# Optimization experiments

Hardware: AMD Instinct MI355X
Metric: run time of the kernel (lower is better)

Reference implementation:

```python
import jax, jax.numpy as jnp
import numpy as np

QK_DIM = 1024
V_DIM = 1024
NUM_HEADS = 16
HEAD_DIM = 64
INNER = NUM_HEADS * HEAD_DIM  # 1024
SCALE = HEAD_DIM ** -0.5


def setup_inputs() -> dict:
    key = jax.random.key(0)
    ks = jax.random.split(key, 8)
    m, nq, nkv = 4, 2048, 2048
    xq = jax.random.normal(ks[0], (m, nq, QK_DIM), dtype=jnp.float32)
    xk = jax.random.normal(ks[1], (m, nkv, QK_DIM), dtype=jnp.float32)
    xv = jax.random.normal(ks[2], (m, nkv, V_DIM), dtype=jnp.float32)
    # torch nn.Linear weights are [out, in]; y = x @ W.T
    s_qk = (QK_DIM) ** -0.5
    s_in = (INNER) ** -0.5
    Wq = jax.random.uniform(ks[3], (INNER, QK_DIM), jnp.float32, -s_qk, s_qk)
    Wk = jax.random.uniform(ks[4], (INNER, QK_DIM), jnp.float32, -s_qk, s_qk)
    Wv = jax.random.uniform(ks[5], (INNER, V_DIM), jnp.float32, -s_qk, s_qk)
    Wo = jax.random.uniform(ks[6], (V_DIM, INNER), jnp.float32, -s_in, s_in)
    bo = jax.random.uniform(ks[7], (V_DIM,), jnp.float32, -s_in, s_in)
    return {"xq": xq, "xk": xk, "xv": xv, "Wq": Wq, "Wk": Wk, "Wv": Wv, "Wo": Wo, "bo": bo}


def reference(xq, xk, xv, Wq, Wk, Wv, Wo, bo):
    m, nq, _ = xq.shape
    nkv = xk.shape[1]
    # projections (no bias), split heads: b n (h d) -> b h n d
    q = (xq @ Wq.T).reshape(m, nq, NUM_HEADS, HEAD_DIM).transpose(0, 2, 1, 3)
    k = (xk @ Wk.T).reshape(m, nkv, NUM_HEADS, HEAD_DIM).transpose(0, 2, 1, 3)
    v = (xv @ Wv.T).reshape(m, nkv, NUM_HEADS, HEAD_DIM).transpose(0, 2, 1, 3)
    dots = jnp.einsum("bhqd,bhkd->bhqk", q, k) * SCALE  # [m,h,nq,nkv]
    attn = jax.nn.softmax(dots, axis=-1)
    out = jnp.einsum("bhqk,bhkd->bhqd", attn, v)
    out = out.transpose(0, 2, 1, 3).reshape(m, nq, INNER)  # b h n d -> b n (h d)
    return out @ Wo.T + bo  # to_out Linear (dropout p=0 -> identity)
```

## Files before the change

### kernel.cpp

```cpp
#include <hip/hip_runtime.h>

typedef unsigned short u16;
using bf16x8 = __attribute__((ext_vector_type(8))) __bf16;
using f32x4  = __attribute__((ext_vector_type(4))) float;

#define QSCALE 0.18033688011f

#define EXP2F(x) __builtin_amdgcn_exp2f(x)

__device__ __forceinline__ u16 f2bf(float f) {
  union { float f; unsigned int u; } x; x.f = f;
  unsigned int r = x.u + 0x7FFFu + ((x.u >> 16) & 1u);
  return (u16)(r >> 16);
}

__device__ __forceinline__ bf16x8 ld8(const u16* p) {
  return *reinterpret_cast<const bf16x8*>(p);
}

__device__ __forceinline__ void gload16(const u16* g, u16* l) {
  __builtin_amdgcn_global_load_lds(
      (const __attribute__((address_space(1))) unsigned int*)g,
      (__attribute__((address_space(3))) unsigned int*)l, 16, 0, 0);
}

__global__ void cast3_f32_to_bf16(const float* __restrict__ a, const float* __restrict__ b,
                                  const float* __restrict__ c, u16* __restrict__ out, int n4) {
  const int y = blockIdx.y;
  const int i = blockIdx.x * 256 + threadIdx.x;
  if (i >= n4) return;
  const float* src = (y == 0) ? a : (y == 1) ? b : c;
  const float4 v = reinterpret_cast<const float4*>(src)[i];
  ushort4 o;
  o.x = f2bf(v.x); o.y = f2bf(v.y); o.z = f2bf(v.z); o.w = f2bf(v.w);
  reinterpret_cast<ushort4*>(out + (size_t)y * n4 * 4)[i] = o;
}

__global__ void cast4_f32_to_bf16(const float* __restrict__ a, const float* __restrict__ b,
                                  const float* __restrict__ c, const float* __restrict__ d,
                                  u16* __restrict__ out, int n4) {
  const int y = blockIdx.y;
  const int i = blockIdx.x * 256 + threadIdx.x;
  if (i >= n4) return;
  const float* src = (y == 0) ? a : (y == 1) ? b : (y == 2) ? c : d;
  const float4 v = reinterpret_cast<const float4*>(src)[i];
  ushort4 o;
  o.x = f2bf(v.x); o.y = f2bf(v.y); o.z = f2bf(v.z); o.w = f2bf(v.w);
  reinterpret_cast<ushort4*>(out + (size_t)y * n4 * 4)[i] = o;
}

#define GEMM_CORE(A_, B_, K_, BX_, BY_)                                              \
  __shared__ alignas(16) u16 lds_a[128 * 32];                                        \
  __shared__ alignas(16) u16 lds_b[128 * 32];                                        \
  const int t = threadIdx.x;                                                         \
  const int w = t >> 6, lane = t & 63;                                               \
  const int wr = w >> 1, wc = w & 1;                                                 \
  const size_t row0 = (size_t)(BY_) * 128;                                           \
  const size_t col0 = (size_t)(BX_) * 128;                                           \
  f32x4 acc[4][4];                                                                   \
  _Pragma("unroll") for (int i = 0; i < 4; ++i)                                      \
    _Pragma("unroll") for (int j = 0; j < 4; ++j) acc[i][j] = {0.f, 0.f, 0.f, 0.f};  \
  const u16* ga = A_ + (row0 + (t >> 2)) * K_ + (t & 3) * 8;                         \
  const u16* gb = B_ + (col0 + (t >> 2)) * K_ + (t & 3) * 8;                         \
  u16* la = lds_a + w * 512;                                                         \
  u16* lb = lds_b + w * 512;                                                         \
  const int fr = lane & 15;                                                          \
  const int fk = (lane >> 4) * 8;                                                    \
  for (int kt = 0; kt < K_; kt += 32) {                                              \
    __syncthreads();                                                                 \
    gload16(ga + kt, la);                                                            \
    gload16(ga + (size_t)64 * K_ + kt, la + 2048);                                   \
    gload16(gb + kt, lb);                                                            \
    gload16(gb + (size_t)64 * K_ + kt, lb + 2048);                                   \
    __syncthreads();                                                                 \
    bf16x8 af[4], bfr[4];                                                            \
    _Pragma("unroll") for (int i = 0; i < 4; ++i)                                    \
      af[i] = ld8(&lds_a[(wr * 64 + i * 16 + fr) * 32 + fk]);                        \
    _Pragma("unroll") for (int j = 0; j < 4; ++j)                                    \
      bfr[j] = ld8(&lds_b[(wc * 64 + j * 16 + fr) * 32 + fk]);                       \
    _Pragma("unroll") for (int i = 0; i < 4; ++i)                                    \
      _Pragma("unroll") for (int j = 0; j < 4; ++j)                                  \
        acc[i][j] = __builtin_amdgcn_mfma_f32_16x16x32_bf16(af[i], bfr[j], acc[i][j], 0, 0, 0); \
  }                                                                                  \
  const int er = (lane >> 4) * 4, ec = lane & 15;

__global__ __launch_bounds__(256)
void gemm_qkv(const u16* __restrict__ Aall, const u16* __restrict__ Ball,
              u16* __restrict__ Call) {
  const int g = (blockIdx.x & 7) * 192 + (blockIdx.x >> 3);
  const int bx = g & 7, by = (g >> 3) & 63, z = g >> 9;
  const u16* A = Aall + (size_t)z * 8192 * 1024;
  const u16* B = Ball + (size_t)z * 1024 * 1024;
  u16* C = Call + (size_t)z * 8192 * 1024;
  GEMM_CORE(A, B, 1024, bx, by)
#pragma unroll
  for (int i = 0; i < 4; ++i)
#pragma unroll
    for (int j = 0; j < 4; ++j) {
      const size_t row = row0 + wr * 64 + i * 16 + er;
      const size_t col = col0 + wc * 64 + j * 16 + ec;
      if (z == 0) {
#pragma unroll
        for (int r = 0; r < 4; ++r)
          C[(row + r) * 1024 + col] = f2bf(acc[i][j][r] * QSCALE);
      } else if (z == 1) {
#pragma unroll
        for (int r = 0; r < 4; ++r)
          C[(row + r) * 1024 + col] = f2bf(acc[i][j][r]);
      } else {
        ushort4 o4;
        o4.x = f2bf(acc[i][j][0]); o4.y = f2bf(acc[i][j][1]);
        o4.z = f2bf(acc[i][j][2]); o4.w = f2bf(acc[i][j][3]);
        const size_t nloc = row & 2047;
        const size_t pos = (nloc & ~(size_t)31) | (((nloc >> 2) & 3) << 3) |
                           (((nloc >> 4) & 1) << 2) | (nloc & 3);
        const size_t idx = (((row >> 11) * 16 + (col >> 6)) * 64 + (col & 63)) * 2048 + pos;
        *reinterpret_cast<ushort4*>(&C[idx]) = o4;
      }
    }
}

__global__ __launch_bounds__(256)
void gemm_out(const u16* __restrict__ A, const u16* __restrict__ B,
              float* __restrict__ Cf, const float* __restrict__ bias) {
  const int g = (blockIdx.x & 7) * 64 + (blockIdx.x >> 3);
  const int bx = g & 7, by = g >> 3;
  GEMM_CORE(A, B, 1024, bx, by)
#pragma unroll
  for (int i = 0; i < 4; ++i)
#pragma unroll
    for (int j = 0; j < 4; ++j) {
      const size_t row = row0 + wr * 64 + i * 16 + er;
      const size_t col = col0 + wc * 64 + j * 16 + ec;
#pragma unroll
      for (int r = 0; r < 4; ++r)
        Cf[(row + r) * 1024 + col] = acc[i][j][r] + bias[col];
    }
}

__global__ __launch_bounds__(256)
void flash_attn(const u16* __restrict__ Q, const u16* __restrict__ Km,
                const u16* __restrict__ Vt, u16* __restrict__ O) {
  const int o_blk = (blockIdx.x & 7) * 128 + (blockIdx.x >> 3);
  const int qt = o_blk & 15, h = (o_blk >> 4) & 15, b = o_blk >> 8;
  const int t = threadIdx.x;
  const int w = t >> 6, lane = t & 63;
  const int l16 = lane & 15, lh = lane >> 4;

  __shared__ alignas(16) u16 kt_lds[2][64][72];
  __shared__ alignas(16) u16 vt_lds[2][64][72];

  const size_t base_qk = ((size_t)b * 2048) * 1024 + (size_t)h * 64;
  const size_t base_vt = ((size_t)(b * 16 + h)) * 64 * 2048;

  bf16x8 qf[2][2];
#pragma unroll
  for (int g = 0; g < 2; ++g) {
    const size_t qrow = (size_t)qt * 128 + (w * 2 + g) * 16 + l16;
    const u16* qp = Q + base_qk + qrow * 1024 + lh * 8;
    qf[g][0] = ld8(qp);
    qf[g][1] = ld8(qp + 32);
  }

  bf16x8 vones;
#pragma unroll
  for (int i = 0; i < 8; ++i) vones[i] = (__bf16)1.0f;

  f32x4 o_acc[2][4];
  f32x4 o_sum[2];
#pragma unroll
  for (int g = 0; g < 2; ++g) {
#pragma unroll
    for (int j = 0; j < 4; ++j) o_acc[g][j] = {0.f, 0.f, 0.f, 0.f};
    o_sum[g] = {0.f, 0.f, 0.f, 0.f};
  }

  const int sr = t >> 2;
  const int sc = (t & 3) * 16;
  const u16* kg = Km + base_qk + (size_t)sr * 1024 + sc;
  const u16* vg = Vt + base_vt + (size_t)sr * 2048 + sc;

  {
    uint4 k0 = *reinterpret_cast<const uint4*>(kg);
    uint4 k1 = *reinterpret_cast<const uint4*>(kg + 8);
    uint4 v0 = *reinterpret_cast<const uint4*>(vg);
    uint4 v1 = *reinterpret_cast<const uint4*>(vg + 8);
    *reinterpret_cast<uint4*>(&kt_lds[0][sr][sc]) = k0;
    *reinterpret_cast<uint4*>(&kt_lds[0][sr][sc + 8]) = k1;
    *reinterpret_cast<uint4*>(&vt_lds[0][sr][sc]) = v0;
    *reinterpret_cast<uint4*>(&vt_lds[0][sr][sc + 8]) = v1;
  }

  for (int it = 0; it < 32; ++it) {
    const int cur = it & 1;
    __syncthreads();

    const int nkv = ((it + 1) & 31) * 64;
    const u16* kp = kg + (size_t)nkv * 1024;
    uint4 kr0 = *reinterpret_cast<const uint4*>(kp);
    uint4 kr1 = *reinterpret_cast<const uint4*>(kp + 8);
    uint4 vr0 = *reinterpret_cast<const uint4*>(vg + nkv);
    uint4 vr1 = *reinterpret_cast<const uint4*>(vg + nkv + 8);

    f32x4 s[2][4];
#pragma unroll
    for (int g = 0; g < 2; ++g)
#pragma unroll
      for (int j = 0; j < 4; ++j) s[g][j] = {0.f, 0.f, 0.f, 0.f};
    __builtin_amdgcn_s_setprio(1);
#pragma unroll
    for (int j = 0; j < 4; ++j)
#pragma unroll
      for (int ks = 0; ks < 2; ++ks) {
        bf16x8 kf = ld8(&kt_lds[cur][j * 16 + l16][ks * 32 + lh * 8]);
        s[0][j] = __builtin_amdgcn_mfma_f32_16x16x32_bf16(kf, qf[0][ks], s[0][j], 0, 0, 0);
        s[1][j] = __builtin_amdgcn_mfma_f32_16x16x32_bf16(kf, qf[1][ks], s[1][j], 0, 0, 0);
      }
    __builtin_amdgcn_s_setprio(0);

    bf16x8 pa[2][2];
#pragma unroll
    for (int g = 0; g < 2; ++g)
#pragma unroll
      for (int j = 0; j < 4; ++j)
#pragma unroll
        for (int r = 0; r < 4; ++r)
          s[g][j][r] = EXP2F(s[g][j][r]);
#pragma unroll
    for (int g = 0; g < 2; ++g)
#pragma unroll
      for (int c = 0; c < 2; ++c)
#pragma unroll
        for (int i = 0; i < 8; ++i)
          pa[g][c][i] = (__bf16)s[g][2 * c + (i >> 2)][i & 3];

    __builtin_amdgcn_s_setprio(1);
#pragma unroll
    for (int c = 0; c < 2; ++c) {
      o_sum[0] = __builtin_amdgcn_mfma_f32_16x16x32_bf16(pa[0][c], vones, o_sum[0], 0, 0, 0);
      o_sum[1] = __builtin_amdgcn_mfma_f32_16x16x32_bf16(pa[1][c], vones, o_sum[1], 0, 0, 0);
#pragma unroll
      for (int jd = 0; jd < 4; ++jd) {
        bf16x8 vf = ld8(&vt_lds[cur][jd * 16 + l16][c * 32 + lh * 8]);
        o_acc[0][jd] = __builtin_amdgcn_mfma_f32_16x16x32_bf16(pa[0][c], vf, o_acc[0][jd], 0, 0, 0);
        o_acc[1][jd] = __builtin_amdgcn_mfma_f32_16x16x32_bf16(pa[1][c], vf, o_acc[1][jd], 0, 0, 0);
      }
    }
    __builtin_amdgcn_s_setprio(0);

    *reinterpret_cast<uint4*>(&kt_lds[cur ^ 1][sr][sc]) = kr0;
    *reinterpret_cast<uint4*>(&kt_lds[cur ^ 1][sr][sc + 8]) = kr1;
    *reinterpret_cast<uint4*>(&vt_lds[cur ^ 1][sr][sc]) = vr0;
    *reinterpret_cast<uint4*>(&vt_lds[cur ^ 1][sr][sc + 8]) = vr1;
  }

#pragma unroll
  for (int g = 0; g < 2; ++g) {
    float linv[4];
#pragma unroll
    for (int r = 0; r < 4; ++r) linv[r] = 1.0f / o_sum[g][r];
    const size_t orow0 = (size_t)b * 2048 + (size_t)qt * 128 + (w * 2 + g) * 16;
#pragma unroll
    for (int jd = 0; jd < 4; ++jd) {
      const int col = h * 64 + jd * 16 + l16;
#pragma unroll
      for (int r = 0; r < 4; ++r)
        O[(orow0 + lh * 4 + r) * 1024 + col] = f2bf(o_acc[g][jd][r] * linv[r]);
    }
  }
}

extern "C" void kernel_launch(void* const* d_in, const int* in_sizes, int n_in,
                              void* d_out, int out_size, void* d_ws, size_t ws_size,
                              hipStream_t stream) {
  const float* xq = (const float*)d_in[0];
  const float* xk = (const float*)d_in[1];
  const float* xv = (const float*)d_in[2];
  const float* Wq = (const float*)d_in[3];
  const float* Wk = (const float*)d_in[4];
  const float* Wv = (const float*)d_in[5];
  const float* Wo = (const float*)d_in[6];
  const float* bo = (const float*)d_in[7];
  float* out = (float*)d_out;

  const size_t X = (size_t)8192 * 1024;
  const size_t W = (size_t)1024 * 1024;

  u16* p = (u16*)d_ws;
  u16* x_bf  = p; p += 3 * X;
  u16* w_bf  = p; p += 4 * W;
  u16* qkv   = p; p += 3 * X;
  u16* attn_bf = x_bf;

  dim3 blk(256);
  cast3_f32_to_bf16<<<dim3(8192, 3), blk, 0, stream>>>(xq, xk, xv, x_bf, (int)(X / 4));
  cast4_f32_to_bf16<<<dim3(1024, 4), blk, 0, stream>>>(Wq, Wk, Wv, Wo, w_bf, (int)(W / 4));

  gemm_qkv<<<dim3(1536), blk, 0, stream>>>(x_bf, w_bf, qkv);

  flash_attn<<<dim3(1024), blk, 0, stream>>>(qkv, qkv + X, qkv + 2 * X, attn_bf);

  gemm_out<<<dim3(512), blk, 0, stream>>>(attn_bf, w_bf + 3 * W, out, bo);
}
```

Measured before the change: 213.8 us.

## Use async global-to-LDS loads with XOR-swizzled K/V layout and larger attention blocks

The QKV GEMM epilogue now writes K and transposed V with an XOR swizzle on the 8-element chunk index. This lets flash attention fill unpadded LDS tiles with direct global_load_lds copies and still read them without bank conflicts. The old register-staged prefetch and LDS store are dropped. Attention blocks grow to 512 threads covering 256 query rows, halving the grid so each K/V tile is reused across more queries, at the cost of fewer blocks and heavier per-block sync.

```diff
diff --git a/kernel.cpp b/kernel.cpp
--- a/kernel.cpp
+++ b/kernel.cpp
@@ -105,16 +105,22 @@
           C[(row + r) * 1024 + col] = f2bf(acc[i][j][r] * QSCALE);
       } else if (z == 1) {
 #pragma unroll
-        for (int r = 0; r < 4; ++r)
-          C[(row + r) * 1024 + col] = f2bf(acc[i][j][r]);
+        for (int r = 0; r < 4; ++r) {
+          const size_t n = row + r;
+          const size_t colswz = (col & ~(size_t)63) |
+                                ((col & 63) ^ (((n & 7) << 3)));
+          C[n * 1024 + colswz] = f2bf(acc[i][j][r]);
+        }
       } else {
         ushort4 o4;
         o4.x = f2bf(acc[i][j][0]); o4.y = f2bf(acc[i][j][1]);
         o4.z = f2bf(acc[i][j][2]); o4.w = f2bf(acc[i][j][3]);
         const size_t nloc = row & 2047;
-        const size_t pos = (nloc & ~(size_t)31) | (((nloc >> 2) & 3) << 3) |
-                           (((nloc >> 4) & 1) << 2) | (nloc & 3);
-        const size_t idx = (((row >> 11) * 16 + (col >> 6)) * 64 + (col & 63)) * 2048 + pos;
+        const size_t d = col & 63;
+        size_t pos = (nloc & ~(size_t)31) | (((nloc >> 2) & 3) << 3) |
+                     (((nloc >> 4) & 1) << 2) | (nloc & 3);
+        pos ^= (d & 7) << 3;
+        const size_t idx = (((row >> 11) * 16 + (col >> 6)) * 64 + d) * 2048 + pos;
         *reinterpret_cast<ushort4*>(&C[idx]) = o4;
       }
     }
@@ -138,17 +144,17 @@
     }
 }
 
-__global__ __launch_bounds__(256)
+__global__ __launch_bounds__(512)
 void flash_attn(const u16* __restrict__ Q, const u16* __restrict__ Km,
                 const u16* __restrict__ Vt, u16* __restrict__ O) {
-  const int o_blk = (blockIdx.x & 7) * 128 + (blockIdx.x >> 3);
-  const int qt = o_blk & 15, h = (o_blk >> 4) & 15, b = o_blk >> 8;
+  const int o_blk = (blockIdx.x & 7) * 64 + (blockIdx.x >> 3);
+  const int qt = o_blk & 7, h = (o_blk >> 3) & 15, b = o_blk >> 7;
   const int t = threadIdx.x;
   const int w = t >> 6, lane = t & 63;
   const int l16 = lane & 15, lh = lane >> 4;
 
-  __shared__ alignas(16) u16 kt_lds[2][64][72];
-  __shared__ alignas(16) u16 vt_lds[2][64][72];
+  __shared__ alignas(16) u16 kt_lds[2][64][64];
+  __shared__ alignas(16) u16 vt_lds[2][64][64];
 
   const size_t base_qk = ((size_t)b * 2048) * 1024 + (size_t)h * 64;
   const size_t base_vt = ((size_t)(b * 16 + h)) * 64 * 2048;
@@ -156,7 +162,7 @@
   bf16x8 qf[2][2];
 #pragma unroll
   for (int g = 0; g < 2; ++g) {
-    const size_t qrow = (size_t)qt * 128 + (w * 2 + g) * 16 + l16;
+    const size_t qrow = (size_t)qt * 256 + (w * 2 + g) * 16 + l16;
     const u16* qp = Q + base_qk + qrow * 1024 + lh * 8;
     qf[g][0] = ld8(qp);
     qf[g][1] = ld8(qp + 32);
@@ -175,32 +181,29 @@
     o_sum[g] = {0.f, 0.f, 0.f, 0.f};
   }
 
-  const int sr = t >> 2;
-  const int sc = (t & 3) * 16;
-  const u16* kg = Km + base_qk + (size_t)sr * 1024 + sc;
-  const u16* vg = Vt + base_vt + (size_t)sr * 2048 + sc;
-
-  {
-    uint4 k0 = *reinterpret_cast<const uint4*>(kg);
-    uint4 k1 = *reinterpret_cast<const uint4*>(kg + 8);
-    uint4 v0 = *reinterpret_cast<const uint4*>(vg);
-    uint4 v1 = *reinterpret_cast<const uint4*>(vg + 8);
-    *reinterpret_cast<uint4*>(&kt_lds[0][sr][sc]) = k0;
-    *reinterpret_cast<uint4*>(&kt_lds[0][sr][sc + 8]) = k1;
-    *reinterpret_cast<uint4*>(&vt_lds[0][sr][sc]) = v0;
-    *reinterpret_cast<uint4*>(&vt_lds[0][sr][sc + 8]) = v1;
-  }
+  const int srow = t >> 3;
+  const int schk = (t & 7) * 8;
+  const u16* kg = Km + base_qk + (size_t)srow * 1024 + schk;
+  const u16* vg = Vt + base_vt + (size_t)srow * 2048 + schk;
+  u16* kl0 = &kt_lds[0][0][0] + w * 512;
+  u16* kl1 = &kt_lds[1][0][0] + w * 512;
+  u16* vl0 = &vt_lds[0][0][0] + w * 512;
+  u16* vl1 = &vt_lds[1][0][0] + w * 512;
+
+  gload16(kg, kl0);
+  gload16(vg, vl0);
+
+  const int xo = (l16 & 7) << 3;
 
   for (int it = 0; it < 32; ++it) {
     const int cur = it & 1;
     __syncthreads();
 
-    const int nkv = ((it + 1) & 31) * 64;
-    const u16* kp = kg + (size_t)nkv * 1024;
-    uint4 kr0 = *reinterpret_cast<const uint4*>(kp);
-    uint4 kr1 = *reinterpret_cast<const uint4*>(kp + 8);
-    uint4 vr0 = *reinterpret_cast<const uint4*>(vg + nkv);
-    uint4 vr1 = *reinterpret_cast<const uint4*>(vg + nkv + 8);
+    if (it != 31) {
+      const int nkv = (it + 1) * 64;
+      gload16(kg + (size_t)nkv * 1024, cur ? kl0 : kl1);
+      gload16(vg + nkv, cur ? vl0 : vl1);
+    }
 
     f32x4 s[2][4];
 #pragma unroll
@@ -212,7 +215,7 @@
     for (int j = 0; j < 4; ++j)
 #pragma unroll
       for (int ks = 0; ks < 2; ++ks) {
-        bf16x8 kf = ld8(&kt_lds[cur][j * 16 + l16][ks * 32 + lh * 8]);
+        bf16x8 kf = ld8(&kt_lds[cur][j * 16 + l16][(ks * 32 + lh * 8) ^ xo]);
         s[0][j] = __builtin_amdgcn_mfma_f32_16x16x32_bf16(kf, qf[0][ks], s[0][j], 0, 0, 0);
         s[1][j] = __builtin_amdgcn_mfma_f32_16x16x32_bf16(kf, qf[1][ks], s[1][j], 0, 0, 0);
       }
@@ -241,17 +244,12 @@
       o_sum[1] = __builtin_amdgcn_mfma_f32_16x16x32_bf16(pa[1][c], vones, o_sum[1], 0, 0, 0);
 #pragma unroll
       for (int jd = 0; jd < 4; ++jd) {
-        bf16x8 vf = ld8(&vt_lds[cur][jd * 16 + l16][c * 32 + lh * 8]);
+        bf16x8 vf = ld8(&vt_lds[cur][jd * 16 + l16][(c * 32 + lh * 8) ^ xo]);
         o_acc[0][jd] = __builtin_amdgcn_mfma_f32_16x16x32_bf16(pa[0][c], vf, o_acc[0][jd], 0, 0, 0);
         o_acc[1][jd] = __builtin_amdgcn_mfma_f32_16x16x32_bf16(pa[1][c], vf, o_acc[1][jd], 0, 0, 0);
       }
     }
     __builtin_amdgcn_s_setprio(0);
-
-    *reinterpret_cast<uint4*>(&kt_lds[cur ^ 1][sr][sc]) = kr0;
-    *reinterpret_cast<uint4*>(&kt_lds[cur ^ 1][sr][sc + 8]) = kr1;
-    *reinterpret_cast<uint4*>(&vt_lds[cur ^ 1][sr][sc]) = vr0;
-    *reinterpret_cast<uint4*>(&vt_lds[cur ^ 1][sr][sc + 8]) = vr1;
   }
 
 #pragma unroll
@@ -259,7 +257,7 @@
     float linv[4];
 #pragma unroll
     for (int r = 0; r < 4; ++r) linv[r] = 1.0f / o_sum[g][r];
-    const size_t orow0 = (size_t)b * 2048 + (size_t)qt * 128 + (w * 2 + g) * 16;
+    const size_t orow0 = (size_t)b * 2048 + (size_t)qt * 256 + (w * 2 + g) * 16;
 #pragma unroll
     for (int jd = 0; jd < 4; ++jd) {
       const int col = h * 64 + jd * 16 + l16;
@@ -298,7 +296,7 @@
 
   gemm_qkv<<<dim3(1536), blk, 0, stream>>>(x_bf, w_bf, qkv);
 
-  flash_attn<<<dim3(1024), blk, 0, stream>>>(qkv, qkv + X, qkv + 2 * X, attn_bf);
+  flash_attn<<<dim3(512), dim3(512), 0, stream>>>(qkv, qkv + X, qkv + 2 * X, attn_bf);
 
   gemm_out<<<dim3(512), blk, 0, stream>>>(attn_bf, w_bf + 3 * W, out, bo);
 }
```

Result: faster. 193.9 us (-9.3%).
